# Optimization experiments

Hardware: AMD Instinct MI355X
Metric: run time of the kernel (lower is better)

The kernel has to match this reference:

```python
import jax, jax.numpy as jnp
import numpy as np

DT = 0.001
TAU_SYN = 0.01
TAU_MEM = 0.005
THRESHOLD = 1.0
ALPHA = float(np.exp(-DT / TAU_SYN))  # syn decay
BETA = float(np.exp(-DT / TAU_MEM))   # mem decay

BATCH, IN_SIZE, OUT_SIZE = 4096, 2048, 2048


@jax.custom_vjp
def spike(x):
    # Heaviside forward with sigmoid-derivative surrogate gradient
    return (x > 0).astype(x.dtype)

def _spike_fwd(x):
    return spike(x), x

def _spike_bwd(x, g):
    s = jax.nn.sigmoid(x)
    return (g * s * (1.0 - s),)

spike.defvjp(_spike_fwd, _spike_bwd)


def setup_inputs() -> dict:
    key = jax.random.key(0)
    k1, k2, k3, k4, k5 = jax.random.split(key, 5)
    inputs = jax.random.normal(k1, (BATCH, IN_SIZE), dtype=jnp.float32)
    I = jax.random.normal(k2, (BATCH, OUT_SIZE), dtype=jnp.float32)
    V = jax.random.normal(k3, (BATCH, OUT_SIZE), dtype=jnp.float32)
    Z = jnp.zeros((BATCH, OUT_SIZE), dtype=jnp.float32)
    # initialize_weights_: ndim<=2 -> normal init
    fwd_w = jax.random.normal(k4, (IN_SIZE, OUT_SIZE), dtype=jnp.float32)
    rec_w = jax.random.normal(k5, (OUT_SIZE, OUT_SIZE), dtype=jnp.float32)
    return {"inputs": inputs, "I": I, "V": V, "Z": Z,
            "fwd_w": fwd_w, "rec_w": rec_w}


def reference(inputs, I, V, Z, fwd_w, rec_w):
    # LIFLayer.forward_Erme, single timestep
    input_current = jnp.matmul(inputs, fwd_w)          # [B, O]
    rec_current = jnp.matmul(Z, rec_w)                 # [B, O]
    is_active = 1.0 - jax.lax.stop_gradient(Z)
    next_I = ALPHA * I + input_current + rec_current
    next_V = (BETA * V + next_I) * is_active
    next_Z = spike(next_V - THRESHOLD)
    return next_Z, next_I, next_V
```

## Files before the change

kernel.cpp:

```cpp
#include <hip/hip_runtime.h>
#include <cstdint>
#include <cstddef>

typedef __bf16 bf16_t;
typedef __bf16 bf16x4 __attribute__((ext_vector_type(4)));
typedef __bf16 bf16x8 __attribute__((ext_vector_type(8)));
typedef float f32x4 __attribute__((ext_vector_type(4)));

#define M_DIM 4096
#define K_DIM 2048
#define N_DIM 2048

#define BM 128
#define BN 128
#define BK 32
#define KT (K_DIM / BK)
#define A_EL (BM * BK)
#define B_EL (BN * BK)
#define PER_BUF (A_EL + B_EL)
#define B_OFF A_EL

#define ZCAP 64

#define MFMA16(a, b, c) \
  __builtin_amdgcn_mfma_f32_16x16x32_bf16((a), (b), (c), 0, 0, 0)

__device__ __forceinline__ void gload_lds16(const bf16_t* g, bf16_t* l) {
  __builtin_amdgcn_global_load_lds(
      (const __attribute__((address_space(1))) void*)g,
      (__attribute__((address_space(3))) void*)l, 16, 0, 0);
}

__global__ __launch_bounds__(256) void prepass_all(
    const float* __restrict__ inputs, const float* __restrict__ fwd_w,
    const float* __restrict__ Z, bf16_t* __restrict__ abf,
    bf16_t* __restrict__ wT, int* __restrict__ zcnt, int* __restrict__ zidx,
    float* __restrict__ zval) {
  __shared__ float tile[64][65];
  const int b = blockIdx.x;
  const int t = threadIdx.x;

  if (b < 4096) {
    const size_t base = ((size_t)b * 256 + t) * 8;
    const float4 v0 = *reinterpret_cast<const float4*>(inputs + base);
    const float4 v1 = *reinterpret_cast<const float4*>(inputs + base + 4);
    bf16x8 o;
    o[0] = (bf16_t)v0.x; o[1] = (bf16_t)v0.y;
    o[2] = (bf16_t)v0.z; o[3] = (bf16_t)v0.w;
    o[4] = (bf16_t)v1.x; o[5] = (bf16_t)v1.y;
    o[6] = (bf16_t)v1.z; o[7] = (bf16_t)v1.w;
    *reinterpret_cast<bf16x8*>(abf + base) = o;
  } else if (b < 5120) {
    const int bb = b - 4096;
    const int n0 = (bb & 31) * 64;
    const int k0 = (bb >> 5) * 64;
#pragma unroll
    for (int p = 0; p < 4; ++p) {
      const int r = p * 16 + (t >> 4);
      const int c = (t & 15) * 4;
      const float4 v = *reinterpret_cast<const float4*>(
          &fwd_w[(size_t)(k0 + r) * N_DIM + n0 + c]);
      tile[r][c + 0] = v.x;
      tile[r][c + 1] = v.y;
      tile[r][c + 2] = v.z;
      tile[r][c + 3] = v.w;
    }
    __syncthreads();
#pragma unroll
    for (int p = 0; p < 4; ++p) {
      const int n = p * 16 + (t >> 4);
      const int c = (t & 15) * 4;
      bf16x4 o;
      o[0] = (bf16_t)tile[c + 0][n];
      o[1] = (bf16_t)tile[c + 1][n];
      o[2] = (bf16_t)tile[c + 2][n];
      o[3] = (bf16_t)tile[c + 3][n];
      *reinterpret_cast<bf16x4*>(&wT[(size_t)(n0 + n) * K_DIM + k0 + c]) = o;
    }
  } else {
    const int row = (b - 5120) * 4 + (t >> 6);
    const int lane = t & 63;
    const float* zr = Z + (size_t)row * N_DIM;
    int local = 0;
#pragma unroll
    for (int c = 0; c < 32; c += 4) {
      const f32x4 v = *reinterpret_cast<const f32x4*>(zr + lane * 32 + c);
#pragma unroll
      for (int e = 0; e < 4; ++e) local += (v[e] != 0.0f) ? 1 : 0;
    }
    int pre = local;
#pragma unroll
    for (int d = 1; d < 64; d <<= 1) {
      const int up = __shfl_up(pre, d, 64);
      if (lane >= d) pre += up;
    }
    const int total = __shfl(pre, 63, 64);
    if (lane == 0) zcnt[row] = total;
    if (total > 0 && total <= ZCAP) {
      int wpos = pre - local;
      int* zi = zidx + (size_t)row * ZCAP;
      float* zv = zval + (size_t)row * ZCAP;
      for (int c = lane * 32; c < lane * 32 + 32; ++c) {
        const float v = zr[c];
        if (v != 0.0f) {
          zi[wpos] = c;
          zv[wpos] = v;
          ++wpos;
        }
      }
    }
  }
}

__global__ __launch_bounds__(256, 2) void lif_gemm_3b(
    const bf16_t* __restrict__ A, const bf16_t* __restrict__ W,
    const float* __restrict__ recw,
    const int* __restrict__ zcnt, const int* __restrict__ zidx,
    const float* __restrict__ zval,
    const float* __restrict__ Iin, const float* __restrict__ Vin,
    const float* __restrict__ Zin,
    float* __restrict__ outZ, float* __restrict__ outI,
    float* __restrict__ outV) {
  __shared__ __align__(16) bf16_t lds[3 * PER_BUF];

  const int tid = threadIdx.x;
  const int lane = tid & 63;
  const int wave = tid >> 6;
  const int wm = wave >> 1;
  const int wn = wave & 1;
  const int l15 = lane & 15;
  const int l4 = lane >> 4;

  const int bid = blockIdx.x;
  const int swz = (bid & 7) * 64 + (bid >> 3);
  const int m0 = (swz >> 4) * BM;
  const int n0 = (swz & 15) * BN;

  const int lr = lane >> 2;
  const int sl = lane & 3;
  const bf16_t* aSrc[2];
  const bf16_t* bSrc[2];
  int aDst[2], bDst[2];
#pragma unroll
  for (int i = 0; i < 2; ++i) {
    const int r = wave * 32 + i * 16 + lr;
    const int sg = sl ^ ((r >> 1) & 3);
    aSrc[i] = A + (size_t)(m0 + r) * K_DIM + sg * 8;
    aDst[i] = r * BK + sl * 8;
    bSrc[i] = W + (size_t)(n0 + r) * K_DIM + sg * 8;
    bDst[i] = B_OFF + r * BK + sl * 8;
  }

  const int aphys = l4 ^ ((l15 >> 1) & 3);
  const int aBase = (wm * 64 + l15) * BK + aphys * 8;
  const int bBase = B_OFF + (wn * 64 + l15) * BK + aphys * 8;

  f32x4 acc[4][4];
#pragma unroll
  for (int i = 0; i < 4; ++i)
#pragma unroll
    for (int j = 0; j < 4; ++j)
#pragma unroll
      for (int e = 0; e < 4; ++e) acc[i][j][e] = 0.0f;

#pragma unroll
  for (int i = 0; i < 2; ++i) {
    gload_lds16(aSrc[i], lds + aDst[i]);
    gload_lds16(bSrc[i], lds + bDst[i]);
  }
#pragma unroll
  for (int i = 0; i < 2; ++i) {
    gload_lds16(aSrc[i] + BK, lds + PER_BUF + aDst[i]);
    gload_lds16(bSrc[i] + BK, lds + PER_BUF + bDst[i]);
  }
  asm volatile("s_waitcnt vmcnt(4)" ::: "memory");
  __builtin_amdgcn_sched_barrier(0);
  __builtin_amdgcn_s_barrier();
  __builtin_amdgcn_sched_barrier(0);

  int bt = 0;
  for (int t = 0; t < KT; ++t) {
    bf16_t* bufC = lds + bt * PER_BUF;
    const int sIdx = (bt == 0) ? 2 : bt - 1;
    bf16_t* bufS = lds + sIdx * PER_BUF;

    if (t + 2 < KT) {
      const int kt = (t + 2) * BK;
#pragma unroll
      for (int i = 0; i < 2; ++i) {
        gload_lds16(aSrc[i] + kt, bufS + aDst[i]);
        gload_lds16(bSrc[i] + kt, bufS + bDst[i]);
      }
    }

    bf16x8 af[4], bfr[4];
#pragma unroll
    for (int mi = 0; mi < 4; ++mi)
      af[mi] = *reinterpret_cast<const bf16x8*>(bufC + aBase + mi * 512);
#pragma unroll
    for (int ni = 0; ni < 4; ++ni)
      bfr[ni] = *reinterpret_cast<const bf16x8*>(bufC + bBase + ni * 512);
    asm volatile("s_waitcnt lgkmcnt(0)" ::: "memory");
    __builtin_amdgcn_sched_barrier(0);

    __builtin_amdgcn_s_setprio(1);
#pragma unroll
    for (int mi = 0; mi < 4; ++mi)
#pragma unroll
      for (int ni = 0; ni < 4; ++ni)
        acc[mi][ni] = MFMA16(af[mi], bfr[ni], acc[mi][ni]);
    __builtin_amdgcn_s_setprio(0);
    __builtin_amdgcn_sched_barrier(0);

    if (t + 2 < KT) {
      asm volatile("s_waitcnt vmcnt(4)" ::: "memory");
    } else if (t + 1 < KT) {
      asm volatile("s_waitcnt vmcnt(0)" ::: "memory");
    }
    __builtin_amdgcn_sched_barrier(0);
    __builtin_amdgcn_s_barrier();
    __builtin_amdgcn_sched_barrier(0);

    bt = (bt == 2) ? 0 : bt + 1;
  }

  const float alpha = 0.90483741803595957f;
  const float beta = 0.81873075307798182f;
  float* swp = reinterpret_cast<float*>(lds) + wave * (16 * 66);
  const int er = lane >> 2;
  const int ec = (lane & 3) * 4;

#pragma unroll
  for (int mi = 0; mi < 4; ++mi) {
#pragma unroll
    for (int ni = 0; ni < 4; ++ni)
#pragma unroll
      for (int j = 0; j < 4; ++j)
        swp[(l4 * 4 + j) * 66 + ni * 16 + l15] = acc[mi][ni][j];

    const int row = m0 + wm * 64 + mi * 16 + er;
    const int colb = n0 + wn * 64 + ec;
    const int cnt = zcnt[row];

    f32x4 rec4[4], gate4[4];
#pragma unroll
    for (int cc = 0; cc < 4; ++cc)
#pragma unroll
      for (int e = 0; e < 4; ++e) {
        rec4[cc][e] = 0.0f;
        gate4[cc][e] = 1.0f;
      }
    if (cnt > 0) {
      if (cnt <= ZCAP) {
        const int* zi = zidx + (size_t)row * ZCAP;
        const float* zv = zval + (size_t)row * ZCAP;
        for (int s = 0; s < cnt; ++s) {
          const int o = zi[s];
          const float v = zv[s];
          const float* wr = recw + (size_t)o * N_DIM + colb;
#pragma unroll
          for (int cc = 0; cc < 4; ++cc) {
            const f32x4 wv = *reinterpret_cast<const f32x4*>(wr + cc * 16);
#pragma unroll
            for (int e = 0; e < 4; ++e) {
              rec4[cc][e] += v * wv[e];
              gate4[cc][e] = (o == colb + cc * 16 + e) ? (1.0f - v)
                                                       : gate4[cc][e];
            }
          }
        }
      } else {
        const float* zr = Zin + (size_t)row * N_DIM;
        for (int o = 0; o < N_DIM; ++o) {
          const float v = zr[o];
          if (v != 0.0f) {
            const float* wr = recw + (size_t)o * N_DIM + colb;
#pragma unroll
            for (int cc = 0; cc < 4; ++cc) {
              const f32x4 wv = *reinterpret_cast<const f32x4*>(wr + cc * 16);
#pragma unroll
              for (int e = 0; e < 4; ++e) {
                rec4[cc][e] += v * wv[e];
                gate4[cc][e] = (o == colb + cc * 16 + e) ? (1.0f - v)
                                                         : gate4[cc][e];
              }
            }
          }
        }
      }
    }

    const size_t gb = (size_t)row * N_DIM + colb;
#pragma unroll
    for (int cc = 0; cc < 4; ++cc) {
      const f32x4 av =
          *reinterpret_cast<const f32x4*>(swp + er * 66 + ec + cc * 16);
      const f32x4 iv = *reinterpret_cast<const f32x4*>(Iin + gb + cc * 16);
      const f32x4 vv = *reinterpret_cast<const f32x4*>(Vin + gb + cc * 16);
      f32x4 nI, nV, nZ;
#pragma unroll
      for (int e = 0; e < 4; ++e) {
        nI[e] = alpha * iv[e] + av[e] + rec4[cc][e];
        nV[e] = (beta * vv[e] + nI[e]) * gate4[cc][e];
        nZ[e] = (nV[e] > 1.0f) ? 1.0f : 0.0f;
      }
      *reinterpret_cast<f32x4*>(outI + gb + cc * 16) = nI;
      *reinterpret_cast<f32x4*>(outV + gb + cc * 16) = nV;
      *reinterpret_cast<f32x4*>(outZ + gb + cc * 16) = nZ;
    }
  }
}

extern "C" void kernel_launch(void* const* d_in, const int* in_sizes, int n_in,
                              void* d_out, int out_size, void* d_ws,
                              size_t ws_size, hipStream_t stream) {
  const float* inputs = (const float*)d_in[0];
  const float* I = (const float*)d_in[1];
  const float* V = (const float*)d_in[2];
  const float* Z = (const float*)d_in[3];
  const float* fwd_w = (const float*)d_in[4];
  const float* rec_w = (const float*)d_in[5];

  float* outZ = (float*)d_out;
  float* outI = outZ + (size_t)M_DIM * N_DIM;
  float* outV = outI + (size_t)M_DIM * N_DIM;

  bf16_t* abf = (bf16_t*)d_ws;
  bf16_t* wT = (bf16_t*)((char*)d_ws + (size_t)M_DIM * K_DIM * 2);
  char* p = (char*)d_ws + (size_t)M_DIM * K_DIM * 2 + (size_t)N_DIM * K_DIM * 2;
  int* zcnt = (int*)p;
  int* zidx = (int*)(p + M_DIM * 4);
  float* zval = (float*)(p + M_DIM * 4 + (size_t)M_DIM * ZCAP * 4);

  hipLaunchKernelGGL(prepass_all, dim3(6144), dim3(256), 0, stream, inputs,
                     fwd_w, Z, abf, wT, zcnt, zidx, zval);
  hipLaunchKernelGGL(lif_gemm_3b, dim3((M_DIM / BM) * (N_DIM / BN)),
                     dim3(256), 0, stream, abf, wT, rec_w, zcnt, zidx, zval, I,
                     V, Z, outZ, outI, outV);
}
```

Baseline: 93.41 us.

## Split GEMM from LIF epilogue and use single-buffered BK=64 tiles

Splits the fused GEMM+LIF kernel into two kernels. The GEMM kernel now uses one single-buffered LDS tile with BK=64, a new swizzle, plain __syncthreads and 3 blocks per CU, and writes the input current to a bf16 scratch buffer. A separate grid-stride epilogue kernel reads that buffer, applies the sparse recurrent contribution and the LIF update per 4-column chunk. This aims for higher occupancy and a simpler epilogue, at the cost of an extra round trip through global memory, an extra launch, bf16 rounding of the current, and losing the software-pipelined prefetch.

```diff
diff --git a/kernel.cpp b/kernel.cpp
--- a/kernel.cpp
+++ b/kernel.cpp
@@ -13,11 +13,10 @@
 
 #define BM 128
 #define BN 128
-#define BK 32
+#define BK 64
 #define KT (K_DIM / BK)
 #define A_EL (BM * BK)
 #define B_EL (BN * BK)
-#define PER_BUF (A_EL + B_EL)
 #define B_OFF A_EL
 
 #define ZCAP 64
@@ -112,16 +111,10 @@
   }
 }
 
-__global__ __launch_bounds__(256, 2) void lif_gemm_3b(
+__global__ __launch_bounds__(256, 3) void gemm_cur(
     const bf16_t* __restrict__ A, const bf16_t* __restrict__ W,
-    const float* __restrict__ recw,
-    const int* __restrict__ zcnt, const int* __restrict__ zidx,
-    const float* __restrict__ zval,
-    const float* __restrict__ Iin, const float* __restrict__ Vin,
-    const float* __restrict__ Zin,
-    float* __restrict__ outZ, float* __restrict__ outI,
-    float* __restrict__ outV) {
-  __shared__ __align__(16) bf16_t lds[3 * PER_BUF];
+    bf16_t* __restrict__ cur) {
+  __shared__ __align__(16) bf16_t lds[A_EL + B_EL];
 
   const int tid = threadIdx.x;
   const int lane = tid & 63;
@@ -136,24 +129,27 @@
   const int m0 = (swz >> 4) * BM;
   const int n0 = (swz & 15) * BN;
 
-  const int lr = lane >> 2;
-  const int sl = lane & 3;
-  const bf16_t* aSrc[2];
-  const bf16_t* bSrc[2];
-  int aDst[2], bDst[2];
-#pragma unroll
-  for (int i = 0; i < 2; ++i) {
-    const int r = wave * 32 + i * 16 + lr;
-    const int sg = sl ^ ((r >> 1) & 3);
+  const int lr = lane >> 3;
+  const int sg = (lane & 7) ^ lr;
+  const bf16_t* aSrc[4];
+  const bf16_t* bSrc[4];
+  int aDst[4], bDst[4];
+#pragma unroll
+  for (int i = 0; i < 4; ++i) {
+    const int r = wave * 32 + i * 8 + lr;
     aSrc[i] = A + (size_t)(m0 + r) * K_DIM + sg * 8;
-    aDst[i] = r * BK + sl * 8;
+    aDst[i] = r * BK + (lane & 7) * 8;
     bSrc[i] = W + (size_t)(n0 + r) * K_DIM + sg * 8;
-    bDst[i] = B_OFF + r * BK + sl * 8;
-  }
-
-  const int aphys = l4 ^ ((l15 >> 1) & 3);
-  const int aBase = (wm * 64 + l15) * BK + aphys * 8;
-  const int bBase = B_OFF + (wn * 64 + l15) * BK + aphys * 8;
+    bDst[i] = B_OFF + r * BK + (lane & 7) * 8;
+  }
+
+  int aBase[2], bBase[2];
+#pragma unroll
+  for (int ks = 0; ks < 2; ++ks) {
+    const int phys = (l4 + ks * 4) ^ (l15 & 7);
+    aBase[ks] = (wm * 64 + l15) * BK + phys * 8;
+    bBase[ks] = B_OFF + (wn * 64 + l15) * BK + phys * 8;
+  }
 
   f32x4 acc[4][4];
 #pragma unroll
@@ -163,73 +159,41 @@
 #pragma unroll
       for (int e = 0; e < 4; ++e) acc[i][j][e] = 0.0f;
 
-#pragma unroll
-  for (int i = 0; i < 2; ++i) {
-    gload_lds16(aSrc[i], lds + aDst[i]);
-    gload_lds16(bSrc[i], lds + bDst[i]);
-  }
-#pragma unroll
-  for (int i = 0; i < 2; ++i) {
-    gload_lds16(aSrc[i] + BK, lds + PER_BUF + aDst[i]);
-    gload_lds16(bSrc[i] + BK, lds + PER_BUF + bDst[i]);
-  }
-  asm volatile("s_waitcnt vmcnt(4)" ::: "memory");
-  __builtin_amdgcn_sched_barrier(0);
-  __builtin_amdgcn_s_barrier();
-  __builtin_amdgcn_sched_barrier(0);
-
-  int bt = 0;
   for (int t = 0; t < KT; ++t) {
-    bf16_t* bufC = lds + bt * PER_BUF;
-    const int sIdx = (bt == 0) ? 2 : bt - 1;
-    bf16_t* bufS = lds + sIdx * PER_BUF;
-
-    if (t + 2 < KT) {
-      const int kt = (t + 2) * BK;
-#pragma unroll
-      for (int i = 0; i < 2; ++i) {
-        gload_lds16(aSrc[i] + kt, bufS + aDst[i]);
-        gload_lds16(bSrc[i] + kt, bufS + bDst[i]);
+    const int kt = t * BK;
+#pragma unroll
+    for (int i = 0; i < 4; ++i) {
+      gload_lds16(aSrc[i] + kt, lds + aDst[i]);
+      gload_lds16(bSrc[i] + kt, lds + bDst[i]);
+    }
+    __syncthreads();
+
+    bf16x8 af[4][2], bfr[4][2];
+#pragma unroll
+    for (int mi = 0; mi < 4; ++mi)
+#pragma unroll
+      for (int ks = 0; ks < 2; ++ks)
+        af[mi][ks] =
+            *reinterpret_cast<const bf16x8*>(lds + aBase[ks] + mi * 1024);
+#pragma unroll
+    for (int ni = 0; ni < 4; ++ni)
+#pragma unroll
+      for (int ks = 0; ks < 2; ++ks)
+        bfr[ni][ks] =
+            *reinterpret_cast<const bf16x8*>(lds + bBase[ks] + ni * 1024);
+#pragma unroll
+    for (int mi = 0; mi < 4; ++mi)
+#pragma unroll
+      for (int ni = 0; ni < 4; ++ni) {
+        acc[mi][ni] = MFMA16(af[mi][0], bfr[ni][0], acc[mi][ni]);
+        acc[mi][ni] = MFMA16(af[mi][1], bfr[ni][1], acc[mi][ni]);
       }
-    }
-
-    bf16x8 af[4], bfr[4];
-#pragma unroll
-    for (int mi = 0; mi < 4; ++mi)
-      af[mi] = *reinterpret_cast<const bf16x8*>(bufC + aBase + mi * 512);
-#pragma unroll
-    for (int ni = 0; ni < 4; ++ni)
-      bfr[ni] = *reinterpret_cast<const bf16x8*>(bufC + bBase + ni * 512);
-    asm volatile("s_waitcnt lgkmcnt(0)" ::: "memory");
-    __builtin_amdgcn_sched_barrier(0);
-
-    __builtin_amdgcn_s_setprio(1);
-#pragma unroll
-    for (int mi = 0; mi < 4; ++mi)
-#pragma unroll
-      for (int ni = 0; ni < 4; ++ni)
-        acc[mi][ni] = MFMA16(af[mi], bfr[ni], acc[mi][ni]);
-    __builtin_amdgcn_s_setprio(0);
-    __builtin_amdgcn_sched_barrier(0);
-
-    if (t + 2 < KT) {
-      asm volatile("s_waitcnt vmcnt(4)" ::: "memory");
-    } else if (t + 1 < KT) {
-      asm volatile("s_waitcnt vmcnt(0)" ::: "memory");
-    }
-    __builtin_amdgcn_sched_barrier(0);
-    __builtin_amdgcn_s_barrier();
-    __builtin_amdgcn_sched_barrier(0);
-
-    bt = (bt == 2) ? 0 : bt + 1;
-  }
-
-  const float alpha = 0.90483741803595957f;
-  const float beta = 0.81873075307798182f;
+    __syncthreads();
+  }
+
   float* swp = reinterpret_cast<float*>(lds) + wave * (16 * 66);
   const int er = lane >> 2;
   const int ec = (lane & 3) * 4;
-
 #pragma unroll
   for (int mi = 0; mi < 4; ++mi) {
 #pragma unroll
@@ -240,16 +204,49 @@
 
     const int row = m0 + wm * 64 + mi * 16 + er;
     const int colb = n0 + wn * 64 + ec;
+    bf16_t* cr = cur + (size_t)row * N_DIM + colb;
+#pragma unroll
+    for (int cc = 0; cc < 4; ++cc) {
+      const f32x4 av =
+          *reinterpret_cast<const f32x4*>(swp + er * 66 + ec + cc * 16);
+      bf16x4 o;
+#pragma unroll
+      for (int e = 0; e < 4; ++e) o[e] = (bf16_t)av[e];
+      *reinterpret_cast<bf16x4*>(cr + cc * 16) = o;
+    }
+    __syncthreads();
+  }
+}
+
+__global__ __launch_bounds__(256) void lif_epi(
+    const bf16_t* __restrict__ cur, const float* __restrict__ recw,
+    const int* __restrict__ zcnt, const int* __restrict__ zidx,
+    const float* __restrict__ zval,
+    const float* __restrict__ Iin, const float* __restrict__ Vin,
+    const float* __restrict__ Zin,
+    float* __restrict__ outZ, float* __restrict__ outI,
+    float* __restrict__ outV) {
+  const float alpha = 0.90483741803595957f;
+  const float beta = 0.81873075307798182f;
+  const int nthr = gridDim.x * 256;
+  const int total = (M_DIM * N_DIM) / 4;
+
+  for (int c = blockIdx.x * 256 + threadIdx.x; c < total; c += nthr) {
+    const int row = c >> 9;
+    const int col = (c & 511) * 4;
+    const size_t gb = (size_t)row * N_DIM + col;
+
+    const bf16x4 cb = *reinterpret_cast<const bf16x4*>(cur + gb);
+    const f32x4 iv = *reinterpret_cast<const f32x4*>(Iin + gb);
+    const f32x4 vv = *reinterpret_cast<const f32x4*>(Vin + gb);
+
+    f32x4 rec, gate;
+#pragma unroll
+    for (int e = 0; e < 4; ++e) {
+      rec[e] = 0.0f;
+      gate[e] = 1.0f;
+    }
     const int cnt = zcnt[row];
-
-    f32x4 rec4[4], gate4[4];
-#pragma unroll
-    for (int cc = 0; cc < 4; ++cc)
-#pragma unroll
-      for (int e = 0; e < 4; ++e) {
-        rec4[cc][e] = 0.0f;
-        gate4[cc][e] = 1.0f;
-      }
     if (cnt > 0) {
       if (cnt <= ZCAP) {
         const int* zi = zidx + (size_t)row * ZCAP;
@@ -257,16 +254,12 @@
         for (int s = 0; s < cnt; ++s) {
           const int o = zi[s];
           const float v = zv[s];
-          const float* wr = recw + (size_t)o * N_DIM + colb;
-#pragma unroll
-          for (int cc = 0; cc < 4; ++cc) {
-            const f32x4 wv = *reinterpret_cast<const f32x4*>(wr + cc * 16);
-#pragma unroll
-            for (int e = 0; e < 4; ++e) {
-              rec4[cc][e] += v * wv[e];
-              gate4[cc][e] = (o == colb + cc * 16 + e) ? (1.0f - v)
-                                                       : gate4[cc][e];
-            }
+          const f32x4 wv =
+              *reinterpret_cast<const f32x4*>(recw + (size_t)o * N_DIM + col);
+#pragma unroll
+          for (int e = 0; e < 4; ++e) {
+            rec[e] += v * wv[e];
+            gate[e] = (o == col + e) ? (1.0f - v) : gate[e];
           }
         }
       } else {
@@ -274,40 +267,28 @@
         for (int o = 0; o < N_DIM; ++o) {
           const float v = zr[o];
           if (v != 0.0f) {
-            const float* wr = recw + (size_t)o * N_DIM + colb;
-#pragma unroll
-            for (int cc = 0; cc < 4; ++cc) {
-              const f32x4 wv = *reinterpret_cast<const f32x4*>(wr + cc * 16);
-#pragma unroll
-              for (int e = 0; e < 4; ++e) {
-                rec4[cc][e] += v * wv[e];
-                gate4[cc][e] = (o == colb + cc * 16 + e) ? (1.0f - v)
-                                                         : gate4[cc][e];
-              }
+            const f32x4 wv = *reinterpret_cast<const f32x4*>(
+                recw + (size_t)o * N_DIM + col);
+#pragma unroll
+            for (int e = 0; e < 4; ++e) {
+              rec[e] += v * wv[e];
+              gate[e] = (o == col + e) ? (1.0f - v) : gate[e];
             }
           }
         }
       }
     }
 
-    const size_t gb = (size_t)row * N_DIM + colb;
-#pragma unroll
-    for (int cc = 0; cc < 4; ++cc) {
-      const f32x4 av =
-          *reinterpret_cast<const f32x4*>(swp + er * 66 + ec + cc * 16);
-      const f32x4 iv = *reinterpret_cast<const f32x4*>(Iin + gb + cc * 16);
-      const f32x4 vv = *reinterpret_cast<const f32x4*>(Vin + gb + cc * 16);
-      f32x4 nI, nV, nZ;
-#pragma unroll
-      for (int e = 0; e < 4; ++e) {
-        nI[e] = alpha * iv[e] + av[e] + rec4[cc][e];
-        nV[e] = (beta * vv[e] + nI[e]) * gate4[cc][e];
-        nZ[e] = (nV[e] > 1.0f) ? 1.0f : 0.0f;
-      }
-      *reinterpret_cast<f32x4*>(outI + gb + cc * 16) = nI;
-      *reinterpret_cast<f32x4*>(outV + gb + cc * 16) = nV;
-      *reinterpret_cast<f32x4*>(outZ + gb + cc * 16) = nZ;
-    }
+    f32x4 nI, nV, nZ;
+#pragma unroll
+    for (int e = 0; e < 4; ++e) {
+      nI[e] = alpha * iv[e] + (float)cb[e] + rec[e];
+      nV[e] = (beta * vv[e] + nI[e]) * gate[e];
+      nZ[e] = (nV[e] > 1.0f) ? 1.0f : 0.0f;
+    }
+    *reinterpret_cast<f32x4*>(outI + gb) = nI;
+    *reinterpret_cast<f32x4*>(outV + gb) = nV;
+    *reinterpret_cast<f32x4*>(outZ + gb) = nZ;
   }
 }
 
@@ -331,10 +312,12 @@
   int* zcnt = (int*)p;
   int* zidx = (int*)(p + M_DIM * 4);
   float* zval = (float*)(p + M_DIM * 4 + (size_t)M_DIM * ZCAP * 4);
+  bf16_t* curb = (bf16_t*)(p + M_DIM * 4 + (size_t)M_DIM * ZCAP * 8);
 
   hipLaunchKernelGGL(prepass_all, dim3(6144), dim3(256), 0, stream, inputs,
                      fwd_w, Z, abf, wT, zcnt, zidx, zval);
-  hipLaunchKernelGGL(lif_gemm_3b, dim3((M_DIM / BM) * (N_DIM / BN)),
-                     dim3(256), 0, stream, abf, wT, rec_w, zcnt, zidx, zval, I,
-                     V, Z, outZ, outI, outV);
-}
+  hipLaunchKernelGGL(gemm_cur, dim3((M_DIM / BM) * (N_DIM / BN)), dim3(256), 0,
+                     stream, abf, wT, curb);
+  hipLaunchKernelGGL(lif_epi, dim3(2048), dim3(256), 0, stream, curb, rec_w,
+                     zcnt, zidx, zval, I, V, Z, outZ, outI, outV);
+}
```

Result: no change. 94.62 us (+1.3%).
